# Kernel optimization log

Measured on AMD Instinct MI355X. Metric: run time of the kernel, lower is better.

## Reference

```python
import jax, jax.numpy as jnp
import numpy as np

N_SIDE = 8
N_PATCHES = 24
W_NORMALS = 1.0
W_PLANAR = 1.0
W_COLLISION = 0.01
W_TEMPLATE = 1.0
W_SYMMETRY = 0.0
SIGMA = 0.1

_lin = np.linspace(0.0, 1.0, N_SIDE).astype(np.float32)
_S, _T = np.meshgrid(_lin, _lin, indexing='ij')
S_GRID = jnp.asarray(_S.flatten())
T_GRID = jnp.asarray(_T.flatten())

def _build_topology():
    n = N_SIDE
    tris = []
    for i in range(n - 1):
        for j in range(n - 1):
            v00 = i * n + j; v10 = (i + 1) * n + j
            v01 = i * n + j + 1; v11 = (i + 1) * n + j + 1
            tris.append([v00, v10, v01]); tris.append([v10, v11, v01])
    tris = np.array(tris, dtype=np.int32)
    edges_pts = np.array([
        [i * n + 0 for i in range(n)],        # edge 0: t=0
        [(n - 1) * n + j for j in range(n)],  # edge 1: s=1
        [i * n + (n - 1) for i in range(n)],  # edge 2: t=1
        [0 * n + j for j in range(n)],        # edge 3: s=0
    ], dtype=np.int32)
    edges_tris = []
    for e in edges_pts:
        es = set(int(x) for x in e)
        et = [ti for ti, t in enumerate(tris) if len(es.intersection(int(v) for v in t)) >= 2]
        edges_tris.append(et[: n - 1])
    return tris, edges_pts, np.array(edges_tris, dtype=np.int32)

TRIANGULATION, GRID_POINT_EDGES, TRIANGULATION_EDGES = _build_topology()

ADJ_PAIRS = [(i, (i + 1) % N_PATCHES, 1) for i in range(N_PATCHES)]
_adjset = set(tuple(sorted((i, (i + 1) % N_PATCHES))) for i in range(N_PATCHES))
NONADJ_PAIRS = [(i, j) for i in range(N_PATCHES) for j in range(i + 1, N_PATCHES)
                if (i, j) not in _adjset]


def _bez_basis(u):
    return jnp.stack([(1 - u) ** 3, 3 * u * (1 - u) ** 2, 3 * u ** 2 * (1 - u), u ** 3], -1)


def coons_sample(s, t, patches):
    """patches [b,P,12,3] cubic-Bezier loop; returns [b,P,M,3]."""
    cp = patches
    c0 = cp[..., 0:4, :]
    c1 = cp[..., 3:7, :]
    c2 = cp[..., 6:10, :]
    c3 = jnp.concatenate([cp[..., 9:12, :], cp[..., 0:1, :]], axis=-2)
    cb = jnp.einsum('mk,bpkc->bpmc', _bez_basis(s), c0)
    cr = jnp.einsum('mk,bpkc->bpmc', _bez_basis(t), c1)
    ct = jnp.einsum('mk,bpkc->bpmc', _bez_basis(1 - s), c2)
    cl = jnp.einsum('mk,bpkc->bpmc', _bez_basis(1 - t), c3)
    P00 = cp[..., 0, :][:, :, None]; P10 = cp[..., 3, :][:, :, None]
    P11 = cp[..., 6, :][:, :, None]; P01 = cp[..., 9, :][:, :, None]
    s_ = s[None, None, :, None]; t_ = t[None, None, :, None]
    ruled = (1 - t_) * cb + t_ * ct + (1 - s_) * cl + s_ * cr
    bil = ((1 - s_) * (1 - t_) * P00 + s_ * (1 - t_) * P10
           + s_ * t_ * P11 + (1 - s_) * t_ * P01)
    return ruled - bil


def _pt_tri_sqdist(p, a, b, c):
    ab = b - a; ac = c - a; ap = p - a
    d1 = jnp.sum(ab * ap, -1); d2 = jnp.sum(ac * ap, -1)
    bp = p - b; d3 = jnp.sum(ab * bp, -1); d4 = jnp.sum(ac * bp, -1)
    cp = p - c; d5 = jnp.sum(ab * cp, -1); d6 = jnp.sum(ac * cp, -1)
    vc = d1 * d4 - d3 * d2; vb = d5 * d2 - d1 * d6; va = d3 * d6 - d5 * d4
    eps = 1e-12
    safe = lambda x: jnp.where(jnp.abs(x) < eps, eps, x)
    t_ab = jnp.clip(d1 / safe(d1 - d3), 0, 1)[..., None]
    t_ac = jnp.clip(d2 / safe(d2 - d6), 0, 1)[..., None]
    t_bc = jnp.clip((d4 - d3) / safe((d4 - d3) + (d5 - d6)), 0, 1)[..., None]
    denom = safe(va + vb + vc)
    v = (vb / denom)[..., None]; w = (vc / denom)[..., None]
    close = a + ab * v + ac * w
    close = jnp.where(((va <= 0) & ((d4 - d3) >= 0) & ((d5 - d6) >= 0))[..., None], b + (c - b) * t_bc, close)
    close = jnp.where(((vb <= 0) & (d2 >= 0) & (d6 <= 0))[..., None], a + ac * t_ac, close)
    close = jnp.where(((d6 >= 0) & (d5 <= d6))[..., None], c, close)
    close = jnp.where(((vc <= 0) & (d1 >= 0) & (d3 <= 0))[..., None], a + ab * t_ab, close)
    close = jnp.where(((d3 >= 0) & (d4 <= d3))[..., None], b, close)
    close = jnp.where(((d1 <= 0) & (d2 <= 0))[..., None], a, close)
    return jnp.sum((p - close) ** 2, -1)


def d_points_to_tris(points, tris):
    """points [K,P,3], tris [K,T,3,3] -> min distance per K."""
    p = points[:, :, None, :]
    a = tris[:, None, :, 0, :]; b = tris[:, None, :, 1, :]; c = tris[:, None, :, 2, :]
    d2 = _pt_tri_sqdist(p, a, b, c)  # [K,P,T]
    return jnp.sqrt(jnp.min(d2, axis=(1, 2)) + 1e-12)


def bboxes_intersect(p1, p2):
    """p1 [b,K,P,3], p2 [b,K,Q,3] -> [b,K] bool."""
    mn1 = p1.min(2); mx1 = p1.max(2); mn2 = p2.min(2); mx2 = p2.max(2)
    return jnp.all((mx1 >= mn2) & (mx2 >= mn1), -1)


def compute_chamfer_losses(points, normals, tp, tn):
    d = (jnp.sum(points ** 2, -1)[:, :, None] + jnp.sum(tp ** 2, -1)[:, None, :]
         - 2 * jnp.einsum('bnc,bmc->bnm', points, tp))
    ca = jnp.min(d, 2); ia = jnp.argmin(d, 2)
    cb = jnp.min(d, 1); ib = jnp.argmin(d, 1)
    na = jnp.sum((normals - jnp.take_along_axis(tn, ia[..., None], 1)) ** 2, -1)
    nb = jnp.sum((tn - jnp.take_along_axis(normals, ib[..., None], 1)) ** 2, -1)
    return ca, cb, na, nb


def planar_patch_loss(st, points, mtds):
    """st [M,2], points [b,P,M,3], mtds [b,P,M]: residual of best-fit linear map."""
    A = jnp.concatenate([st, jnp.ones_like(st[:, :1])], 1)  # [M,3]
    AtA = A.T @ A
    sol = jnp.linalg.solve(AtA, jnp.einsum('mk,bpmc->bpkc', A, points))
    res = points - jnp.einsum('mk,bpkc->bpmc', A, sol)
    l = jnp.sum(res ** 2, -1)
    return jnp.mean(jnp.sum(mtds * l, -1) / jnp.sum(mtds, -1))


def _gather2(x, idx):
    """x [b,K,N,...], idx [K,R] -> x gathered along axis 2."""
    full = idx.reshape((1,) + idx.shape + (1,) * (x.ndim - 3))
    full = jnp.broadcast_to(full, x.shape[:2] + (idx.shape[1],) + x.shape[3:])
    return jnp.take_along_axis(x, full, axis=2)


def _forward(target, patches, points, normals, mtds, st, template_normals):
    b, n_patches = patches.shape[0], patches.shape[1]
    target_points = target[:, :, :3]
    target_normals = target[:, :, 3:]
    pts_flat = points.reshape(b, -1, 3)
    nrm_flat = normals.reshape(b, -1, 3)
    mtds_flat = mtds.reshape(b, -1)

    ca, cb, na, nb = compute_chamfer_losses(pts_flat, nrm_flat, target_points, target_normals)
    ca = jnp.sum(mtds_flat * ca, -1) / jnp.sum(mtds_flat, -1)
    cb = cb.mean(1)
    chamfer_loss = ((ca + cb).mean() / 2).reshape(1)
    na = jnp.sum(mtds_flat * na, -1) / jnp.sum(mtds_flat, -1)
    nb = nb.mean(-1)
    normals_loss = ((na + nb).mean() / 2).reshape(1)

    tnl = jnp.sum((template_normals[None] - normals) ** 2, -1)  # [b,P,M]
    template_normals_loss = (jnp.sum(mtds * tnl, -1) / jnp.sum(mtds, -1)).mean().reshape(1)

    planar_loss = planar_patch_loss(st, points, mtds).reshape(1)

    # ---- collision ----
    tri_idx = jnp.asarray(TRIANGULATION)
    grid_points = coons_sample(S_GRID, T_GRID, patches)       # [b,P,64,3]
    triangles = grid_points[:, :, tri_idx]                    # [b,P,98,3,3]

    i1s, i2s, e1s = zip(*ADJ_PAIRS)
    i1s = np.array(i1s); i2s = np.array(i2s); e1s = np.array(e1s)
    K = len(e1s)
    pts1 = _gather2(grid_points[:, i1s], jnp.asarray(GRID_POINT_EDGES[e1s]))    # [b,K,8,3]
    tris1 = _gather2(triangles[:, i1s], jnp.asarray(TRIANGULATION_EDGES[e1s]))  # [b,K,7,3,3]
    pts2 = grid_points[:, i2s]
    tris2 = triangles[:, i2s]
    mask_adj = bboxes_intersect(pts1, pts2).any(0)  # [K]
    d1 = d_points_to_tris(pts1.reshape(b * K, 8, 3), tris2.reshape(b * K, -1, 3, 3))
    d2 = d_points_to_tris(pts2.reshape(b * K, -1, 3), tris1.reshape(b * K, -1, 3, 3))
    d = jnp.minimum(d1, d2).reshape(b, K)
    col_adj = jnp.where(mask_adj[None, :], jnp.exp(-(d / SIGMA) ** 2), 0.0)

    j1s, j2s = zip(*NONADJ_PAIRS)
    j1s = np.array(j1s); j2s = np.array(j2s)
    Kn = len(j1s)
    p1 = grid_points[:, j1s]; p2 = grid_points[:, j2s]
    t1 = triangles[:, j1s]; t2 = triangles[:, j2s]
    mask_non = bboxes_intersect(p1, p2).any(0)  # [Kn]
    d1 = d_points_to_tris(p1.reshape(b * Kn, -1, 3), t2.reshape(b * Kn, -1, 3, 3))
    d2 = d_points_to_tris(p2.reshape(b * Kn, -1, 3), t1.reshape(b * Kn, -1, 3, 3))
    dn = jnp.minimum(d1, d2).reshape(b, Kn)
    col_non = jnp.where(mask_non[None, :], jnp.exp(-(dn / SIGMA) ** 2), 0.0)

    collision_loss = (col_adj.sum(-1) + col_non.sum(-1)).mean().reshape(1)
    symmetry_loss = jnp.zeros(1, dtype=patches.dtype)

    loss = (chamfer_loss + W_NORMALS * normals_loss + W_COLLISION * collision_loss
            + W_PLANAR * planar_loss + W_TEMPLATE * template_normals_loss
            + W_SYMMETRY * symmetry_loss)
    return (loss, chamfer_loss, normals_loss, collision_loss, planar_loss,
            template_normals_loss, symmetry_loss)


def setup_inputs() -> dict:
    key = jax.random.key(0)
    ks = jax.random.split(key, 7)
    b, P, M, Mt = 4, N_PATCHES, 256, 4096
    return {
        'target': jax.random.normal(ks[0], (b, Mt, 6), jnp.float32),
        'patches': jax.random.normal(ks[1], (b, P, 12, 3), jnp.float32),
        'points': jax.random.normal(ks[2], (b, P, M, 3), jnp.float32),
        'normals': jax.random.normal(ks[3], (b, P, M, 3), jnp.float32),
        'mtds': jax.random.uniform(ks[4], (b, P, M), jnp.float32) + 0.01,
        'st': jax.random.uniform(ks[5], (M, 2), jnp.float32),
        'template_normals': jax.random.normal(ks[6], (P, M, 3), jnp.float32),
    }


def reference(target, patches, points, normals, mtds, st, template_normals):
    return _forward(target, patches, points, normals, mtds, st, template_normals)
```

## Files before the change

### kernel.cpp

```cpp
#include <hip/hip_runtime.h>
#include <math.h>

#define NPATCH 24
#define NB 4
#define MPTS 256
#define MT 4096
#define NPTS (NPATCH*MPTS)
#define GRIDPTS 64
#define SIGMA2INV 100.0f
#define PRUNE_MARGIN 0.45f


__device__ inline unsigned encodeFloat(float f) {
    unsigned u = __float_as_uint(f);
    return (u & 0x80000000u) ? ~u : (u | 0x80000000u);
}
__device__ inline float decodeFloat(unsigned e) {
    return __uint_as_float((e & 0x80000000u) ? (e ^ 0x80000000u) : ~e);
}

__device__ inline unsigned long long waveMinU64(unsigned long long k) {
    for (int o = 32; o > 0; o >>= 1) {
        unsigned long long other = __shfl_xor(k, o);
        k = (other < k) ? other : k;
    }
    return k;
}

template<int NV>
__device__ inline void blockReduceSumN(const float* vals, float* out, float* scratch) {
    int wid = threadIdx.x >> 6, lane = threadIdx.x & 63;
#pragma unroll
    for (int i = 0; i < NV; ++i) {
        float v = vals[i];
        for (int o = 32; o > 0; o >>= 1) v += __shfl_down(v, o);
        if (lane == 0) scratch[wid * NV + i] = v;
    }
    __syncthreads();
    if (threadIdx.x < NV)
        out[threadIdx.x] = scratch[0 * NV + threadIdx.x] + scratch[1 * NV + threadIdx.x] +
                           scratch[2 * NV + threadIdx.x] + scratch[3 * NV + threadIdx.x];
    __syncthreads();
}

__device__ inline float clamp01f(float x) { return fminf(fmaxf(x, 0.0f), 1.0f); }
__device__ inline float safercp(float x) {
    float s = fabsf(x) < 1e-12f ? 1e-12f : x;
    return __builtin_amdgcn_rcpf(s);
}

__device__ inline float ptTriSqDistP(float px, float py, float pz, const float4* T) {
    float4 f0 = T[0], f1 = T[1], f2 = T[2], f3 = T[3];
    float ax = f0.x, ay = f0.y, az = f0.z;
    float abx = f1.x, aby = f1.y, abz = f1.z;
    float acx = f2.x, acy = f2.y, acz = f2.z;
    float abp = abx * px + aby * py + abz * pz;
    float acp = acx * px + acy * py + acz * pz;
    float d1 = abp - f0.w;
    float d2 = acp - f1.w;
    float d3 = abp - f2.w;
    float d4 = acp - f3.x;
    float d5 = abp - f3.y;
    float d6 = acp - f3.z;
    float vc = d1 * d4 - d3 * d2;
    float vb = d5 * d2 - d1 * d6;
    float va = d3 * d6 - d5 * d4;
    float t_ab = clamp01f(d1 * safercp(d1 - d3));
    float t_ac = clamp01f(d2 * safercp(d2 - d6));
    float t_bc = clamp01f((d4 - d3) * safercp((d4 - d3) + (d5 - d6)));
    float rden = safercp(va + vb + vc);
    float v = vb * rden, w = vc * rden;
    float clx = ax + abx * v + acx * w;
    float cly = ay + aby * v + acy * w;
    float clz = az + abz * v + acz * w;
    if (va <= 0.0f && (d4 - d3) >= 0.0f && (d5 - d6) >= 0.0f) {
        clx = (ax + abx) + (acx - abx) * t_bc;
        cly = (ay + aby) + (acy - aby) * t_bc;
        clz = (az + abz) + (acz - abz) * t_bc;
    }
    if (vb <= 0.0f && d2 >= 0.0f && d6 <= 0.0f) {
        clx = ax + acx * t_ac; cly = ay + acy * t_ac; clz = az + acz * t_ac;
    }
    if (d6 >= 0.0f && d5 <= d6) { clx = ax + acx; cly = ay + acy; clz = az + acz; }
    if (vc <= 0.0f && d1 >= 0.0f && d3 <= 0.0f) {
        clx = ax + abx * t_ab; cly = ay + aby * t_ab; clz = az + abz * t_ab;
    }
    if (d3 >= 0.0f && d4 <= d3) { clx = ax + abx; cly = ay + aby; clz = az + abz; }
    if (d1 <= 0.0f && d2 <= 0.0f) { clx = ax; cly = ay; clz = az; }
    float dx = px - clx, dy = py - cly, dz = pz - clz;
    return dx * dx + dy * dy + dz * dz;
}

__global__ __launch_bounds__(128) void k_coons_tri(const float* __restrict__ patches,
                                                   float* __restrict__ grid,
                                                   float* __restrict__ bbF,
                                                   float* __restrict__ bbE,
                                                   float4* __restrict__ TDg,
                                                   float4* __restrict__ TSg,
                                                   unsigned* __restrict__ pairmin,
                                                   float* __restrict__ acc) {
    __shared__ float Pl[192];
    int bp = blockIdx.x;
    int m = threadIdx.x;
    if (bp == 0) {
        for (int i = m; i < 1104; i += 128) pairmin[i] = 0xFFFFFFFFu;
        if (m < 32) acc[m] = 0.0f;
    }
    if (m < 64) {
        int i = m >> 3, j = m & 7;
        float s = (i == 7) ? 1.0f : (float)i * (1.0f / 7.0f);
        float t = (j == 7) ? 1.0f : (float)j * (1.0f / 7.0f);
        const float* cp = patches + bp * 36;
        float bs[4], bt[4], bs1[4], bt1[4];
        {
            float u, vv;
            u = s; vv = 1.0f - u; bs[0] = vv * vv * vv; bs[1] = 3.f * u * vv * vv; bs[2] = 3.f * u * u * vv; bs[3] = u * u * u;
            u = t; vv = 1.0f - u; bt[0] = vv * vv * vv; bt[1] = 3.f * u * vv * vv; bt[2] = 3.f * u * u * vv; bt[3] = u * u * u;
            u = 1.0f - s; vv = 1.0f - u; bs1[0] = vv * vv * vv; bs1[1] = 3.f * u * vv * vv; bs1[2] = 3.f * u * u * vv; bs1[3] = u * u * u;
            u = 1.0f - t; vv = 1.0f - u; bt1[0] = vv * vv * vv; bt1[1] = 3.f * u * vv * vv; bt1[2] = 3.f * u * u * vv; bt1[3] = u * u * u;
        }
        float g[3];
#pragma unroll
        for (int c = 0; c < 3; ++c) {
            float cb = bs[0] * cp[0 * 3 + c] + bs[1] * cp[1 * 3 + c] + bs[2] * cp[2 * 3 + c] + bs[3] * cp[3 * 3 + c];
            float cr = bt[0] * cp[3 * 3 + c] + bt[1] * cp[4 * 3 + c] + bt[2] * cp[5 * 3 + c] + bt[3] * cp[6 * 3 + c];
            float ct = bs1[0] * cp[6 * 3 + c] + bs1[1] * cp[7 * 3 + c] + bs1[2] * cp[8 * 3 + c] + bs1[3] * cp[9 * 3 + c];
            float cl = bt1[0] * cp[9 * 3 + c] + bt1[1] * cp[10 * 3 + c] + bt1[2] * cp[11 * 3 + c] + bt1[3] * cp[0 * 3 + c];
            float P00 = cp[0 * 3 + c], P10 = cp[3 * 3 + c], P11 = cp[6 * 3 + c], P01 = cp[9 * 3 + c];
            float ruled = (1.0f - t) * cb + t * ct + (1.0f - s) * cl + s * cr;
            float bil = (1.0f - s) * (1.0f - t) * P00 + s * (1.0f - t) * P10 + s * t * P11 + (1.0f - s) * t * P01;
            g[c] = ruled - bil;
            grid[(bp * GRIDPTS + m) * 3 + c] = g[c];
            Pl[m * 3 + c] = g[c];
        }
        float mnF[3], mxF[3], mnE[3], mxE[3];
        bool edge = (m >= 56);
#pragma unroll
        for (int c = 0; c < 3; ++c) {
            mnF[c] = g[c]; mxF[c] = g[c];
            mnE[c] = edge ? g[c] : 1e30f;
            mxE[c] = edge ? g[c] : -1e30f;
        }
        for (int o = 32; o > 0; o >>= 1) {
#pragma unroll
            for (int c = 0; c < 3; ++c) {
                mnF[c] = fminf(mnF[c], __shfl_down(mnF[c], o));
                mxF[c] = fmaxf(mxF[c], __shfl_down(mxF[c], o));
                mnE[c] = fminf(mnE[c], __shfl_down(mnE[c], o));
                mxE[c] = fmaxf(mxE[c], __shfl_down(mxE[c], o));
            }
        }
        if (m == 0) {
#pragma unroll
            for (int c = 0; c < 3; ++c) {
                bbF[bp * 6 + c] = mnF[c]; bbF[bp * 6 + 3 + c] = mxF[c];
                bbE[bp * 6 + c] = mnE[c]; bbE[bp * 6 + 3 + c] = mxE[c];
            }
        }
    }
    __syncthreads();
    int t = m;
    if (t < 98) {
        int cell = t >> 1, ii = cell / 7, jj = cell - ii * 7;
        int v00 = ii * 8 + jj;
        int va, vb, vc;
        if (t & 1) { va = v00 + 8; vb = v00 + 9; vc = v00 + 1; }
        else       { va = v00;     vb = v00 + 8; vc = v00 + 1; }
        float ax = Pl[va * 3], ay = Pl[va * 3 + 1], az = Pl[va * 3 + 2];
        float bx = Pl[vb * 3], by = Pl[vb * 3 + 1], bz = Pl[vb * 3 + 2];
        float cx = Pl[vc * 3], cy = Pl[vc * 3 + 1], cz = Pl[vc * 3 + 2];
        float abx = bx - ax, aby = by - ay, abz = bz - az;
        float acx = cx - ax, acy = cy - ay, acz = cz - az;
        float ab_a = abx * ax + aby * ay + abz * az;
        float ac_a = acx * ax + acy * ay + acz * az;
        float ab_b = abx * bx + aby * by + abz * bz;
        float ac_b = acx * bx + acy * by + acz * bz;
        float ab_c = abx * cx + aby * cy + abz * cz;
        float ac_c = acx * cx + acy * cy + acz * cz;
        float4* dst = TDg + ((size_t)bp * 98 + t) * 4;
        dst[0] = make_float4(ax, ay, az, ab_a);
        dst[1] = make_float4(abx, aby, abz, ac_a);
        dst[2] = make_float4(acx, acy, acz, ab_b);
        dst[3] = make_float4(ac_b, ab_c, ac_c, 0.0f);
        float gx = (ax + bx + cx) * (1.0f / 3.0f);
        float gy = (ay + by + cy) * (1.0f / 3.0f);
        float gz = (az + bz + cz) * (1.0f / 3.0f);
        float ra = (ax - gx) * (ax - gx) + (ay - gy) * (ay - gy) + (az - gz) * (az - gz);
        float rb = (bx - gx) * (bx - gx) + (by - gy) * (by - gy) + (bz - gz) * (bz - gz);
        float rc = (cx - gx) * (cx - gx) + (cy - gy) * (cy - gy) + (cz - gz) * (cz - gz);
        float r = sqrtf(fmaxf(ra, fmaxf(rb, rc)));
        TSg[(size_t)bp * 98 + t] = make_float4(gx, gy, gz, r);
    }
}

__global__ __launch_bounds__(256) void k_mega(const float* __restrict__ target,
                                              const float* __restrict__ points,
                                              const float* __restrict__ grid,
                                              const float4* __restrict__ TDg,
                                              const float4* __restrict__ TSg,
                                              const float* __restrict__ bbF,
                                              const float* __restrict__ bbE,
                                              float* __restrict__ pa,
                                              float* __restrict__ pb,
                                              unsigned* __restrict__ pairmin) {
    __shared__ float4 smem[128];
    __shared__ float4 Pts[64];
    __shared__ float4 Sph[98];
    __shared__ unsigned short wl[6272];
    __shared__ int cnt;
    __shared__ float sred[4];
    int id = blockIdx.x;
    int b = blockIdx.y;
    int tid = threadIdx.x;

    if (id >= 528) {
        bool isA = (id < 624);
        int qbase, ch;
        float qx0, qy0, qz0, qx1, qy1, qz1, qx2, qy2, qz2, qx3, qy3, qz3;
        float qx4, qy4, qz4, qx5, qy5, qz5, qx6, qy6, qz6, qx7, qy7, qz7;
        if (isA) {
            int rel = id - 528;
            int qb = rel >> 5; ch = rel & 31;
            qbase = qb * 2048 + tid * 8;
            int chbase = ch * 128;
            if (tid < 128) {
                const float* tp = target + (size_t)(b * MT + chbase + tid) * 6;
                float x = tp[0], y = tp[1], z = tp[2];
                smem[tid] = make_float4(x, y, z, 0.5f * (x * x + y * y + z * z));
            }
            const float4* pf = (const float4*)(points + ((size_t)b * NPTS + qbase) * 3);
            float4 v0 = pf[0], v1 = pf[1], v2 = pf[2], v3 = pf[3], v4 = pf[4], v5 = pf[5];
            qx0 = v0.x; qy0 = v0.y; qz0 = v0.z;
            qx1 = v0.w; qy1 = v1.x; qz1 = v1.y;
            qx2 = v1.z; qy2 = v1.w; qz2 = v2.x;
            qx3 = v2.y; qy3 = v2.z; qz3 = v2.w;
            qx4 = v3.x; qy4 = v3.y; qz4 = v3.z;
            qx5 = v3.w; qy5 = v4.x; qz5 = v4.y;
            qx6 = v4.z; qy6 = v4.w; qz6 = v5.x;
            qx7 = v5.y; qy7 = v5.z; qz7 = v5.w;
        } else {
            int rel = id - 624;
            int qb = rel / 48; ch = rel - qb * 48;
            qbase = qb * 2048 + tid * 8;
            int chbase = ch * 128;
            if (tid < 128) {
                const float* pp = points + (size_t)(b * NPTS + chbase + tid) * 3;
                float x = pp[0], y = pp[1], z = pp[2];
                smem[tid] = make_float4(x, y, z, 0.5f * (x * x + y * y + z * z));
            }
            const float* tf = target + (size_t)(b * MT + qbase) * 6;
            float2 a0 = *(const float2*)(tf + 0);  float z0 = tf[2];
            float2 a1 = *(const float2*)(tf + 6);  float z1 = tf[8];
            float2 a2 = *(const float2*)(tf + 12); float z2 = tf[14];
            float2 a3 = *(const float2*)(tf + 18); float z3 = tf[20];
            float2 a4 = *(const float2*)(tf + 24); float z4 = tf[26];
            float2 a5 = *(const float2*)(tf + 30); float z5 = tf[32];
            float2 a6 = *(const float2*)(tf + 36); float z6 = tf[38];
            float2 a7 = *(const float2*)(tf + 42); float z7 = tf[44];
            qx0 = a0.x; qy0 = a0.y; qz0 = z0;
            qx1 = a1.x; qy1 = a1.y; qz1 = z1;
            qx2 = a2.x; qy2 = a2.y; qz2 = z2;
            qx3 = a3.x; qy3 = a3.y; qz3 = z3;
            qx4 = a4.x; qy4 = a4.y; qz4 = z4;
            qx5 = a5.x; qy5 = a5.y; qz5 = z5;
            qx6 = a6.x; qy6 = a6.y; qz6 = z6;
            qx7 = a7.x; qy7 = a7.y; qz7 = z7;
        }
        __syncthreads();
        float sc0 = 1e30f, sc1 = 1e30f, sc2 = 1e30f, sc3 = 1e30f;
        float sc4 = 1e30f, sc5 = 1e30f, sc6 = 1e30f, sc7 = 1e30f;
#pragma unroll 8
        for (int k = 0; k < 128; ++k) {
            float4 T = smem[k];
            sc0 = fminf(sc0, fmaf(-qx0, T.x, fmaf(-qy0, T.y, fmaf(-qz0, T.z, T.w))));
            sc1 = fminf(sc1, fmaf(-qx1, T.x, fmaf(-qy1, T.y, fmaf(-qz1, T.z, T.w))));
            sc2 = fminf(sc2, fmaf(-qx2, T.x, fmaf(-qy2, T.y, fmaf(-qz2, T.z, T.w))));
            sc3 = fminf(sc3, fmaf(-qx3, T.x, fmaf(-qy3, T.y, fmaf(-qz3, T.z, T.w))));
            sc4 = fminf(sc4, fmaf(-qx4, T.x, fmaf(-qy4, T.y, fmaf(-qz4, T.z, T.w))));
            sc5 = fminf(sc5, fmaf(-qx5, T.x, fmaf(-qy5, T.y, fmaf(-qz5, T.z, T.w))));
            sc6 = fminf(sc6, fmaf(-qx6, T.x, fmaf(-qy6, T.y, fmaf(-qz6, T.z, T.w))));
            sc7 = fminf(sc7, fmaf(-qx7, T.x, fmaf(-qy7, T.y, fmaf(-qz7, T.z, T.w))));
        }
        float* dstp = isA ? (pa + ((size_t)(b * 32 + ch)) * NPTS + qbase)
                          : (pb + ((size_t)(b * 48 + ch)) * MT + qbase);
        *(float4*)(dstp) = make_float4(sc0, sc1, sc2, sc3);
        *(float4*)(dstp + 4) = make_float4(sc4, sc5, sc6, sc7);
        return;
    }

    float best = 1e30f;
    int pairIdx;

    if (id < 24) {
        int pair = id;
        pairIdx = pair;
        int i1 = pair, i2 = (pair + 1) % NPATCH;
        bool mask = false;
        for (int bb = 0; bb < NB; ++bb) {
            const float* B1 = bbE + (bb * NPATCH + i1) * 6;
            const float* B2 = bbF + (bb * NPATCH + i2) * 6;
            bool it = (B1[3] >= B2[0]) && (B2[3] >= B1[0]) &&
                      (B1[4] >= B2[1]) && (B2[4] >= B1[1]) &&
                      (B1[5] >= B2[2]) && (B2[5] >= B1[2]);
            mask |= it;
        }
        if (!mask) return;
        const float* P1 = grid + (size_t)(b * NPATCH + i1) * 192;
        const float* P2 = grid + (size_t)(b * NPATCH + i2) * 192;
        const float4* T1 = TDg + (size_t)(b * NPATCH + i1) * 98 * 4;
        const float4* T2 = TDg + (size_t)(b * NPATCH + i2) * 98 * 4;
        for (int tt = tid; tt < 1232; tt += 256) {
            const float4* T;
            float px, py, pz;
            if (tt < 784) {
                int ptI = tt / 98, tri = tt - ptI * 98;
                const float* gp = P1 + (56 + ptI) * 3;
                px = gp[0]; py = gp[1]; pz = gp[2];
                T = T2 + tri * 4;
            } else {
                int rr = tt - 784;
                int ptI = rr / 7, e = rr - ptI * 7;
                const float* gp = P2 + ptI * 3;
                px = gp[0]; py = gp[1]; pz = gp[2];
                T = T1 + (85 + 2 * e) * 4;
            }
            best = fminf(best, ptTriSqDistP(px, py, pz, T));
        }
    } else {
        int r = id - 24;
        int pi2 = r >> 1, dir = r & 1;
        pairIdx = 24 + pi2;
        int k = pi2, i1 = 0;
        while (i1 < NPATCH) {
            int cnt_ = (i1 == 0) ? 21 : (22 - i1);
            if (k < cnt_) break;
            k -= cnt_; ++i1;
        }
        int i2 = i1 + 2 + k;
        bool mask = false;
        for (int bb = 0; bb < NB; ++bb) {
            const float* B1 = bbF + (bb * NPATCH + i1) * 6;
            const float* B2 = bbF + (bb * NPATCH + i2) * 6;
            bool it = (B1[3] >= B2[0]) && (B2[3] >= B1[0]) &&
                      (B1[4] >= B2[1]) && (B2[4] >= B1[1]) &&
                      (B1[5] >= B2[2]) && (B2[5] >= B1[2]);
            mask |= it;
        }
        if (!mask) return;
        int ip_pts = dir ? i2 : i1;
        int ip_tri = dir ? i1 : i2;
        if (tid < 64) {
            const float* gp = grid + ((size_t)(b * NPATCH + ip_pts) * 64 + tid) * 3;
            Pts[tid] = make_float4(gp[0], gp[1], gp[2], 0.0f);
        } else if (tid < 128) {
            int q = tid - 64;
            const float* gq = grid + ((size_t)(b * NPATCH + ip_tri) * 64 + q) * 3;
            smem[q] = make_float4(gq[0], gq[1], gq[2], 0.0f);
        } else if (tid < 226) {
            int t = tid - 128;
            Sph[t] = TSg[(size_t)(b * NPATCH + ip_tri) * 98 + t];
        }
        if (tid == 0) cnt = 0;
        __syncthreads();
        int pt = tid & 63;
        float4 P = Pts[pt];
        float px = P.x, py = P.y, pz = P.z;
        float ub = 1e30f;
        int o0 = (tid >> 6) * 16;
        for (int q = o0; q < o0 + 16; ++q) {
            float4 Q = smem[q];
            float dx = px - Q.x, dy = py - Q.y, dz = pz - Q.z;
            ub = fminf(ub, dx * dx + dy * dy + dz * dz);
        }
        for (int o = 32; o > 0; o >>= 1) ub = fminf(ub, __shfl_xor(ub, o));
        if ((tid & 63) == 0) sred[tid >> 6] = ub;
        __syncthreads();
        ub = fminf(fminf(sred[0], sred[1]), fminf(sred[2], sred[3]));
        float sB = fminf(sqrtf(ub) + 1e-4f, PRUNE_MARGIN);
        best = ub;
        int lane = tid & 63;
        int wtri = tid >> 6;
        for (int t = wtri; t < 98; t += 4) {
            float4 S = Sph[t];
            float dx = px - S.x, dy = py - S.y, dz = pz - S.z;
            float lb = dx * dx + dy * dy + dz * dz;
            float thr = sB + S.w;
            bool pred = (lb <= thr * thr);
            unsigned long long mb = __ballot(pred);
            if (mb != 0ull) {
                int wbase;
                if (lane == 0) wbase = atomicAdd(&cnt, __popcll(mb));
                wbase = __shfl(wbase, 0);
                if (pred) {
                    int off = __popcll(mb & ((1ull << lane) - 1ull));
                    wl[wbase + off] = (unsigned short)((pt << 7) | t);
                }
            }
        }
        __syncthreads();
        int n = cnt;
        const float4* TD = TDg + (size_t)(b * NPATCH + ip_tri) * 98 * 4;
        for (int i = tid; i < n; i += 256) {
            int w = wl[i];
            int ppt = w >> 7, t = w & 127;
            float4 PP = Pts[ppt];
            best = fminf(best, ptTriSqDistP(PP.x, PP.y, PP.z, TD + t * 4));
        }
        __syncthreads();
    }

    for (int o = 32; o > 0; o >>= 1) best = fminf(best, __shfl_down(best, o));
    if ((tid & 63) == 0) sred[tid >> 6] = best;
    __syncthreads();
    if (tid == 0) {
        float d2 = fminf(fminf(sred[0], sred[1]), fminf(sred[2], sred[3]));
        atomicMin(&pairmin[b * 276 + pairIdx], encodeFloat(d2));
    }
}

__global__ __launch_bounds__(256) void k_argmin(const float* __restrict__ target,
                                                const float* __restrict__ points,
                                                const float* __restrict__ pa,
                                                const float* __restrict__ pb,
                                                unsigned long long* __restrict__ best_a,
                                                unsigned long long* __restrict__ best_b) {
    int w = blockIdx.x * 4 + (threadIdx.x >> 6);
    int lane = threadIdx.x & 63;
    if (w < 24576) {
        int b = w / NPTS, qi = w - b * NPTS;
        float v = (lane < 32) ? pa[((size_t)(b * 32 + lane)) * NPTS + qi] : 1e30f;
        unsigned long long key = ((unsigned long long)encodeFloat(v) << 32) | (unsigned)lane;
        key = waveMinU64(key);
        int minch = (int)(key & 0xffffffffu);
        int base = minch * 128;
        const float* pp = points + ((size_t)b * NPTS + qi) * 3;
        float px = pp[0], py = pp[1], pz = pp[2];
        const float* tb0 = target + (size_t)b * MT * 6;
        unsigned long long bk = 0xFFFFFFFFFFFFFFFFull;
#pragma unroll
        for (int rr = 0; rr < 2; ++rr) {
            int k = base + lane + rr * 64;
            const float* tq = tb0 + (size_t)k * 6;
            float x = tq[0], y = tq[1], z = tq[2];
            float hw = 0.5f * (x * x + y * y + z * z);
            float s = fmaf(-px, x, fmaf(-py, y, fmaf(-pz, z, hw)));
            unsigned long long kk = ((unsigned long long)encodeFloat(s) << 32) | (unsigned)k;
            bk = (kk < bk) ? kk : bk;
        }
        bk = waveMinU64(bk);
        if (lane == 0) best_a[(size_t)b * NPTS + qi] = bk;
    } else {
        int idx = w - 24576;
        int b = idx / MT, mt = idx - b * MT;
        float v = (lane < 48) ? pb[((size_t)(b * 48 + lane)) * MT + mt] : 1e30f;
        unsigned long long key = ((unsigned long long)encodeFloat(v) << 32) | (unsigned)lane;
        key = waveMinU64(key);
        int minch = (int)(key & 0xffffffffu);
        int base = minch * 128;
        const float* tq = target + (size_t)(b * MT + mt) * 6;
        float tx = tq[0], ty = tq[1], tz = tq[2];
        const float* pt0 = points + (size_t)b * NPTS * 3;
        unsigned long long bk = 0xFFFFFFFFFFFFFFFFull;
#pragma unroll
        for (int rr = 0; rr < 2; ++rr) {
            int k = base + lane + rr * 64;
            const float* pp2 = pt0 + (size_t)k * 3;
            float x = pp2[0], y = pp2[1], z = pp2[2];
            float hw = 0.5f * (x * x + y * y + z * z);
            float s = fmaf(-tx, x, fmaf(-ty, y, fmaf(-tz, z, hw)));
            unsigned long long kk = ((unsigned long long)encodeFloat(s) << 32) | (unsigned)k;
            bk = (kk < bk) ? kk : bk;
        }
        bk = waveMinU64(bk);
        if (lane == 0) best_b[(size_t)b * MT + mt] = bk;
    }
}

__global__ __launch_bounds__(256) void k_final(const float* __restrict__ points,
                                               const float* __restrict__ normals,
                                               const float* __restrict__ target,
                                               const float* __restrict__ mtds,
                                               const float* __restrict__ st,
                                               const float* __restrict__ tmpl,
                                               const unsigned long long* __restrict__ best_a,
                                               const unsigned long long* __restrict__ best_b,
                                               float* __restrict__ acc) {
    int id = blockIdx.x, b = blockIdx.y;
    if (id < 24) {
        int p = id;
        int m = threadIdx.x;
        int bp = b * NPATCH + p;
        const float* pp = points + (size_t)(bp * MPTS + m) * 3;
        float px = pp[0], py = pp[1], pz = pp[2];
        float pn = px * px + py * py + pz * pz;
        const float* nr = normals + (size_t)(bp * MPTS + m) * 3;
        float nx = nr[0], ny = nr[1], nz = nr[2];
        float w = mtds[bp * MPTS + m];
        float s = st[2 * m], t = st[2 * m + 1];
        unsigned long long pk = best_a[(size_t)b * NPTS + p * MPTS + m];
        float ca = fmaf(2.0f, decodeFloat((unsigned)(pk >> 32)), pn);
        int ia = (int)(pk & 0xffffffffu);
        const float* tq = target + (size_t)(b * MT + ia) * 6 + 3;
        float dx = nx - tq[0], dy = ny - tq[1], dz = nz - tq[2];
        float na = dx * dx + dy * dy + dz * dz;
        const float* tm = tmpl + (size_t)(p * MPTS + m) * 3;
        float ex = tm[0] - nx, ey = tm[1] - ny, ez = tm[2] - nz;
        float tnl = ex * ex + ey * ey + ez * ez;

        float vals[18];
        vals[0] = w * ca; vals[1] = w * na; vals[2] = w; vals[3] = w * tnl;
        vals[4] = s * px; vals[5] = s * py; vals[6] = s * pz;
        vals[7] = t * px; vals[8] = t * py; vals[9] = t * pz;
        vals[10] = px; vals[11] = py; vals[12] = pz;
        vals[13] = s * s; vals[14] = s * t; vals[15] = s; vals[16] = t * t; vals[17] = t;

        __shared__ float scratch[4 * 18];
        __shared__ float red[18];
        blockReduceSumN<18>(vals, red, scratch);

        __shared__ float sol[9];
        __shared__ float smtd_sh;
        if (threadIdx.x == 0) {
            float a00 = red[13], a01 = red[14], a02 = red[15];
            float a11 = red[16], a12 = red[17], a22 = 256.0f;
            float c00 = a11 * a22 - a12 * a12;
            float c01 = a02 * a12 - a01 * a22;
            float c02 = a01 * a12 - a02 * a11;
            float det = a00 * c00 + a01 * c01 + a02 * c02;
            float idet = 1.0f / det;
            float i00 = c00 * idet, i01 = c01 * idet, i02 = c02 * idet;
            float i11 = (a00 * a22 - a02 * a02) * idet;
            float i12 = (a01 * a02 - a00 * a12) * idet;
            float i22 = (a00 * a11 - a01 * a01) * idet;
#pragma unroll
            for (int c = 0; c < 3; ++c) {
                float b0 = red[4 + c], b1 = red[7 + c], b2 = red[10 + c];
                sol[0 * 3 + c] = i00 * b0 + i01 * b1 + i02 * b2;
                sol[1 * 3 + c] = i01 * b0 + i11 * b1 + i12 * b2;
                sol[2 * 3 + c] = i02 * b0 + i12 * b1 + i22 * b2;
            }
            smtd_sh = red[2];
            atomicAdd(&acc[0 + b], red[0]);
            atomicAdd(&acc[4 + b], red[1]);
            atomicAdd(&acc[8 + b], red[2]);
            atomicAdd(&acc[20], red[3] / red[2]);
        }
        __syncthreads();
        float rx = px - (s * sol[0] + t * sol[3] + sol[6]);
        float ry = py - (s * sol[1] + t * sol[4] + sol[7]);
        float rz = pz - (s * sol[2] + t * sol[5] + sol[8]);
        float v2 = w * (rx * rx + ry * ry + rz * rz);
        for (int o = 32; o > 0; o >>= 1) v2 += __shfl_down(v2, o);
        __shared__ float s2[4];
        if ((threadIdx.x & 63) == 0) s2[threadIdx.x >> 6] = v2;
        __syncthreads();
        if (threadIdx.x == 0)
            atomicAdd(&acc[21], (s2[0] + s2[1] + s2[2] + s2[3]) / smtd_sh);
    } else {
        int mc = id - 24;
        int mt = mc * 256 + threadIdx.x;
        const float* tq = target + (size_t)(b * MT + mt) * 6;
        float tx = tq[0], ty = tq[1], tz = tq[2];
        float tn2 = tx * tx + ty * ty + tz * tz;
        unsigned long long pk = best_b[(size_t)b * MT + mt];
        float cb = fmaf(2.0f, decodeFloat((unsigned)(pk >> 32)), tn2);
        int ib = (int)(pk & 0xffffffffu);
        const float* nr = normals + (size_t)(b * NPTS + ib) * 3;
        float dx = tq[3] - nr[0], dy = tq[4] - nr[1], dz = tq[5] - nr[2];
        float nb = dx * dx + dy * dy + dz * dz;
        float vals[2] = {cb, nb};
        __shared__ float scratchB[4 * 2];
        __shared__ float redB[2];
        blockReduceSumN<2>(vals, redB, scratchB);
        if (threadIdx.x == 0) {
            atomicAdd(&acc[12 + b], redB[0]);
            atomicAdd(&acc[16 + b], redB[1]);
        }
    }
}

__global__ __launch_bounds__(256) void k_finish(const float* __restrict__ acc,
                                                const unsigned* __restrict__ pairmin,
                                                float* __restrict__ out) {
    int tid = threadIdx.x;
    float s = 0.0f;
    for (int idx = tid; idx < 4 * 276; idx += 256) {
        unsigned key = pairmin[idx];
        if (key != 0xFFFFFFFFu) {
            float d2 = decodeFloat(key);
            s += expf(-(d2 + 1e-12f) * SIGMA2INV);
        }
    }
    for (int o = 32; o > 0; o >>= 1) s += __shfl_down(s, o);
    __shared__ float sred[4];
    if ((tid & 63) == 0) sred[tid >> 6] = s;
    __syncthreads();
    if (tid == 0) {
        float col = (sred[0] + sred[1] + sred[2] + sred[3]) * 0.25f;
        float ch = 0.0f, no = 0.0f;
        for (int b = 0; b < NB; ++b) {
            float caw = acc[0 + b] / acc[8 + b];
            float naw = acc[4 + b] / acc[8 + b];
            float cbm = acc[12 + b] / (float)MT;
            float nbm = acc[16 + b] / (float)MT;
            ch += caw + cbm;
            no += naw + nbm;
        }
        ch = ch * 0.25f * 0.5f;
        no = no * 0.25f * 0.5f;
        float tpl = acc[20] / 96.0f;
        float pl = acc[21] / 96.0f;
        float loss = ch + no + 0.01f * col + pl + tpl;
        out[0] = loss;
        out[1] = ch;
        out[2] = no;
        out[3] = col;
        out[4] = pl;
        out[5] = tpl;
        out[6] = 0.0f;
    }
}

extern "C" void kernel_launch(void* const* d_in, const int* in_sizes, int n_in,
                              void* d_out, int out_size, void* d_ws, size_t ws_size,
                              hipStream_t stream) {
    (void)in_sizes; (void)n_in; (void)out_size; (void)ws_size;
    const float* target = (const float*)d_in[0];
    const float* patches = (const float*)d_in[1];
    const float* points = (const float*)d_in[2];
    const float* normals = (const float*)d_in[3];
    const float* mtds = (const float*)d_in[4];
    const float* st = (const float*)d_in[5];
    const float* tmpl = (const float*)d_in[6];
    float* out = (float*)d_out;
    char* ws = (char*)d_ws;

    float* grid = (float*)(ws + 0);
    float* bbF = (float*)(ws + 73728);
    float* bbE = (float*)(ws + 76032);
    unsigned* pairmin = (unsigned*)(ws + 78336);
    float* acc = (float*)(ws + 82752);
    float4* TDg = (float4*)(ws + 82880);
    float4* TSg = (float4*)(ws + 684992);
    float* pa = (float*)(ws + 835520);
    float* pb = (float*)(ws + 3981248);
    unsigned long long* best_a = (unsigned long long*)(ws + 7126976);
    unsigned long long* best_b = (unsigned long long*)(ws + 7323584);

    k_coons_tri<<<dim3(NB * NPATCH), dim3(128), 0, stream>>>(patches, grid, bbF, bbE,
                                                             TDg, TSg, pairmin, acc);
    k_mega<<<dim3(720, NB), dim3(256), 0, stream>>>(target, points, grid, TDg, TSg,
                                                    bbF, bbE, pa, pb, pairmin);
    k_argmin<<<dim3(10240), dim3(256), 0, stream>>>(target, points, pa, pb, best_a, best_b);
    k_final<<<dim3(40, NB), dim3(256), 0, stream>>>(points, normals, target, mtds, st,
                                                    tmpl, best_a, best_b, acc);
    k_finish<<<1, 256, 0, stream>>>(acc, pairmin, out);
}
```

Baseline: 75.32 us.

## Remap argmin to one query per lane, add sphere culling, fuse finish

k_argmin is reorganized so each lane owns one query point and the four waves split the channel scan and the 128-candidate refinement, combining partial results through shared memory. This replaces per-query wave reductions and strided target loads with fewer, coalesced blocks. The collision narrow phase gets a bounding-sphere lower-bound test that skips exact point-triangle distance work when it cannot improve the current minimum. k_finish is folded into k_final using a last-block-done atomic counter, which removes one launch but relies on acc[31] being zeroed beforehand and on correct fencing.

```diff
diff --git a/kernel.cpp b/kernel.cpp
--- a/kernel.cpp
+++ b/kernel.cpp
@@ -17,14 +17,6 @@
 }
 __device__ inline float decodeFloat(unsigned e) {
     return __uint_as_float((e & 0x80000000u) ? (e ^ 0x80000000u) : ~e);
-}
-
-__device__ inline unsigned long long waveMinU64(unsigned long long k) {
-    for (int o = 32; o > 0; o >>= 1) {
-        unsigned long long other = __shfl_xor(k, o);
-        k = (other < k) ? other : k;
-    }
-    return k;
 }
 
 template<int NV>
@@ -404,6 +396,11 @@
             int w = wl[i];
             int ppt = w >> 7, t = w & 127;
             float4 PP = Pts[ppt];
+            float4 S = Sph[t];
+            float dx = PP.x - S.x, dy = PP.y - S.y, dz = PP.z - S.z;
+            float lb = dx * dx + dy * dy + dz * dz;
+            float thr = sqrtf(best) + S.w;
+            if (lb > thr * thr) continue;
             best = fminf(best, ptTriSqDistP(PP.x, PP.y, PP.z, TD + t * 4));
         }
         __syncthreads();
@@ -424,55 +421,102 @@
                                                 const float* __restrict__ pb,
                                                 unsigned long long* __restrict__ best_a,
                                                 unsigned long long* __restrict__ best_b) {
-    int w = blockIdx.x * 4 + (threadIdx.x >> 6);
-    int lane = threadIdx.x & 63;
-    if (w < 24576) {
-        int b = w / NPTS, qi = w - b * NPTS;
-        float v = (lane < 32) ? pa[((size_t)(b * 32 + lane)) * NPTS + qi] : 1e30f;
-        unsigned long long key = ((unsigned long long)encodeFloat(v) << 32) | (unsigned)lane;
-        key = waveMinU64(key);
-        int minch = (int)(key & 0xffffffffu);
-        int base = minch * 128;
-        const float* pp = points + ((size_t)b * NPTS + qi) * 3;
+    __shared__ unsigned long long red[4][64];
+    int blk = blockIdx.x;
+    int tid = threadIdx.x;
+    int lane = tid & 63, grp = tid >> 6;
+    if (blk < 384) {
+        int Q0 = blk * 64;
+        int b = Q0 / NPTS, q0 = Q0 - b * NPTS;
+        int q = q0 + lane;
+        unsigned long long k1 = 0xFFFFFFFFFFFFFFFFull;
+        const float* paB = pa + (size_t)b * 32 * NPTS + q;
+#pragma unroll
+        for (int c = 0; c < 8; ++c) {
+            int ch = grp * 8 + c;
+            float v = paB[(size_t)ch * NPTS];
+            unsigned long long kk = ((unsigned long long)encodeFloat(v) << 32) | (unsigned)ch;
+            k1 = (kk < k1) ? kk : k1;
+        }
+        red[grp][lane] = k1;
+        __syncthreads();
+        unsigned long long m0 = red[0][lane], m1 = red[1][lane];
+        unsigned long long m2 = red[2][lane], m3 = red[3][lane];
+        unsigned long long mm = m0 < m1 ? m0 : m1;
+        mm = m2 < mm ? m2 : mm;
+        mm = m3 < mm ? m3 : mm;
+        int minch = (int)(mm & 0xffffffffu);
+        int base = minch * 128 + grp * 32;
+        const float* pp = points + ((size_t)b * NPTS + q) * 3;
         float px = pp[0], py = pp[1], pz = pp[2];
         const float* tb0 = target + (size_t)b * MT * 6;
         unsigned long long bk = 0xFFFFFFFFFFFFFFFFull;
-#pragma unroll
-        for (int rr = 0; rr < 2; ++rr) {
-            int k = base + lane + rr * 64;
-            const float* tq = tb0 + (size_t)k * 6;
+        for (int c = 0; c < 32; ++c) {
+            int kidx = base + c;
+            const float* tq = tb0 + (size_t)kidx * 6;
             float x = tq[0], y = tq[1], z = tq[2];
             float hw = 0.5f * (x * x + y * y + z * z);
             float s = fmaf(-px, x, fmaf(-py, y, fmaf(-pz, z, hw)));
-            unsigned long long kk = ((unsigned long long)encodeFloat(s) << 32) | (unsigned)k;
+            unsigned long long kk = ((unsigned long long)encodeFloat(s) << 32) | (unsigned)kidx;
             bk = (kk < bk) ? kk : bk;
         }
-        bk = waveMinU64(bk);
-        if (lane == 0) best_a[(size_t)b * NPTS + qi] = bk;
+        __syncthreads();
+        red[grp][lane] = bk;
+        __syncthreads();
+        if (tid < 64) {
+            unsigned long long r0 = red[0][tid], r1 = red[1][tid];
+            unsigned long long r2 = red[2][tid], r3 = red[3][tid];
+            unsigned long long rr = r0 < r1 ? r0 : r1;
+            rr = r2 < rr ? r2 : rr;
+            rr = r3 < rr ? r3 : rr;
+            best_a[(size_t)b * NPTS + q0 + tid] = rr;
+        }
     } else {
-        int idx = w - 24576;
-        int b = idx / MT, mt = idx - b * MT;
-        float v = (lane < 48) ? pb[((size_t)(b * 48 + lane)) * MT + mt] : 1e30f;
-        unsigned long long key = ((unsigned long long)encodeFloat(v) << 32) | (unsigned)lane;
-        key = waveMinU64(key);
-        int minch = (int)(key & 0xffffffffu);
-        int base = minch * 128;
+        int Q0 = (blk - 384) * 64;
+        int b = Q0 / MT, m0q = Q0 - b * MT;
+        int mt = m0q + lane;
+        unsigned long long k1 = 0xFFFFFFFFFFFFFFFFull;
+        const float* pbB = pb + (size_t)b * 48 * MT + mt;
+#pragma unroll
+        for (int c = 0; c < 12; ++c) {
+            int ch = grp * 12 + c;
+            float v = pbB[(size_t)ch * MT];
+            unsigned long long kk = ((unsigned long long)encodeFloat(v) << 32) | (unsigned)ch;
+            k1 = (kk < k1) ? kk : k1;
+        }
+        red[grp][lane] = k1;
+        __syncthreads();
+        unsigned long long m0 = red[0][lane], m1 = red[1][lane];
+        unsigned long long m2 = red[2][lane], m3 = red[3][lane];
+        unsigned long long mm = m0 < m1 ? m0 : m1;
+        mm = m2 < mm ? m2 : mm;
+        mm = m3 < mm ? m3 : mm;
+        int minch = (int)(mm & 0xffffffffu);
+        int base = minch * 128 + grp * 32;
         const float* tq = target + (size_t)(b * MT + mt) * 6;
         float tx = tq[0], ty = tq[1], tz = tq[2];
         const float* pt0 = points + (size_t)b * NPTS * 3;
         unsigned long long bk = 0xFFFFFFFFFFFFFFFFull;
-#pragma unroll
-        for (int rr = 0; rr < 2; ++rr) {
-            int k = base + lane + rr * 64;
-            const float* pp2 = pt0 + (size_t)k * 3;
+        for (int c = 0; c < 32; ++c) {
+            int kidx = base + c;
+            const float* pp2 = pt0 + (size_t)kidx * 3;
             float x = pp2[0], y = pp2[1], z = pp2[2];
             float hw = 0.5f * (x * x + y * y + z * z);
             float s = fmaf(-tx, x, fmaf(-ty, y, fmaf(-tz, z, hw)));
-            unsigned long long kk = ((unsigned long long)encodeFloat(s) << 32) | (unsigned)k;
+            unsigned long long kk = ((unsigned long long)encodeFloat(s) << 32) | (unsigned)kidx;
             bk = (kk < bk) ? kk : bk;
         }
-        bk = waveMinU64(bk);
-        if (lane == 0) best_b[(size_t)b * MT + mt] = bk;
+        __syncthreads();
+        red[grp][lane] = bk;
+        __syncthreads();
+        if (tid < 64) {
+            unsigned long long r0 = red[0][tid], r1 = red[1][tid];
+            unsigned long long r2 = red[2][tid], r3 = red[3][tid];
+            unsigned long long rr = r0 < r1 ? r0 : r1;
+            rr = r2 < rr ? r2 : rr;
+            rr = r3 < rr ? r3 : rr;
+            best_b[(size_t)b * MT + m0q + tid] = rr;
+        }
     }
 }
 
@@ -484,7 +528,11 @@
                                                const float* __restrict__ tmpl,
                                                const unsigned long long* __restrict__ best_a,
                                                const unsigned long long* __restrict__ best_b,
-                                               float* __restrict__ acc) {
+                                               float* __restrict__ acc,
+                                               unsigned* __restrict__ pairmin,
+                                               float* __restrict__ out) {
+    __shared__ float finred[4];
+    __shared__ int lastFlag;
     int id = blockIdx.x, b = blockIdx.y;
     if (id < 24) {
         int p = id;
@@ -577,39 +625,44 @@
             atomicAdd(&acc[16 + b], redB[1]);
         }
     }
-}
-
-__global__ __launch_bounds__(256) void k_finish(const float* __restrict__ acc,
-                                                const unsigned* __restrict__ pairmin,
-                                                float* __restrict__ out) {
+
+    __syncthreads();
+    if (threadIdx.x == 0) {
+        __threadfence();
+        unsigned done = atomicAdd((unsigned*)acc + 31, 1u) + 1u;
+        lastFlag = (done == 160u) ? 1 : 0;
+    }
+    __syncthreads();
+    if (!lastFlag) return;
+    __threadfence();
     int tid = threadIdx.x;
     float s = 0.0f;
     for (int idx = tid; idx < 4 * 276; idx += 256) {
-        unsigned key = pairmin[idx];
+        unsigned key = atomicOr(&pairmin[idx], 0u);
         if (key != 0xFFFFFFFFu) {
             float d2 = decodeFloat(key);
             s += expf(-(d2 + 1e-12f) * SIGMA2INV);
         }
     }
     for (int o = 32; o > 0; o >>= 1) s += __shfl_down(s, o);
-    __shared__ float sred[4];
-    if ((tid & 63) == 0) sred[tid >> 6] = s;
+    if ((tid & 63) == 0) finred[tid >> 6] = s;
     __syncthreads();
     if (tid == 0) {
-        float col = (sred[0] + sred[1] + sred[2] + sred[3]) * 0.25f;
+        float col = (finred[0] + finred[1] + finred[2] + finred[3]) * 0.25f;
         float ch = 0.0f, no = 0.0f;
-        for (int b = 0; b < NB; ++b) {
-            float caw = acc[0 + b] / acc[8 + b];
-            float naw = acc[4 + b] / acc[8 + b];
-            float cbm = acc[12 + b] / (float)MT;
-            float nbm = acc[16 + b] / (float)MT;
-            ch += caw + cbm;
-            no += naw + nbm;
+        for (int bb = 0; bb < NB; ++bb) {
+            float sa = atomicAdd(&acc[0 + bb], 0.0f);
+            float sna = atomicAdd(&acc[4 + bb], 0.0f);
+            float sw = atomicAdd(&acc[8 + bb], 0.0f);
+            float scb = atomicAdd(&acc[12 + bb], 0.0f);
+            float snb = atomicAdd(&acc[16 + bb], 0.0f);
+            ch += sa / sw + scb / (float)MT;
+            no += sna / sw + snb / (float)MT;
         }
         ch = ch * 0.25f * 0.5f;
         no = no * 0.25f * 0.5f;
-        float tpl = acc[20] / 96.0f;
-        float pl = acc[21] / 96.0f;
+        float tpl = atomicAdd(&acc[20], 0.0f) / 96.0f;
+        float pl = atomicAdd(&acc[21], 0.0f) / 96.0f;
         float loss = ch + no + 0.01f * col + pl + tpl;
         out[0] = loss;
         out[1] = ch;
@@ -651,8 +704,7 @@
                                                              TDg, TSg, pairmin, acc);
     k_mega<<<dim3(720, NB), dim3(256), 0, stream>>>(target, points, grid, TDg, TSg,
                                                     bbF, bbE, pa, pb, pairmin);
-    k_argmin<<<dim3(10240), dim3(256), 0, stream>>>(target, points, pa, pb, best_a, best_b);
+    k_argmin<<<dim3(640), dim3(256), 0, stream>>>(target, points, pa, pb, best_a, best_b);
     k_final<<<dim3(40, NB), dim3(256), 0, stream>>>(points, normals, target, mtds, st,
-                                                    tmpl, best_a, best_b, acc);
-    k_finish<<<1, 256, 0, stream>>>(acc, pairmin, out);
-}
+                                                    tmpl, best_a, best_b, acc, pairmin, out);
+}
```

Measured after the change: 79.66 us. 5.8% more time.

## Derive target-to-point column minima from point-to-target distance tiles

Applied to the files above, without the earlier changes.

The chamfer partial-min blocks now compute the point-to-target distance tile once and obtain both directions from it. Row minima stay in registers, and column minima come from a 16-lane shuffle reduction stored in a shared buffer aliased with the worklist. This removes the separate 96 target-query blocks per batch. The cost is extra shuffles and min operations in the inner loop, plus a second shared-memory write-out phase.

```diff
diff --git a/kernel.cpp b/kernel.cpp
--- a/kernel.cpp
+++ b/kernel.cpp
@@ -206,85 +206,71 @@
     __shared__ float4 smem[128];
     __shared__ float4 Pts[64];
     __shared__ float4 Sph[98];
-    __shared__ unsigned short wl[6272];
     __shared__ int cnt;
     __shared__ float sred[4];
+    __shared__ __attribute__((aligned(16))) unsigned char poolbuf[12544];
+    float (*colsh)[132] = (float(*)[132])poolbuf;
+    unsigned short* wl = (unsigned short*)poolbuf;
     int id = blockIdx.x;
     int b = blockIdx.y;
     int tid = threadIdx.x;
 
     if (id >= 528) {
-        bool isA = (id < 624);
-        int qbase, ch;
-        float qx0, qy0, qz0, qx1, qy1, qz1, qx2, qy2, qz2, qx3, qy3, qz3;
-        float qx4, qy4, qz4, qx5, qy5, qz5, qx6, qy6, qz6, qx7, qy7, qz7;
-        if (isA) {
-            int rel = id - 528;
-            int qb = rel >> 5; ch = rel & 31;
-            qbase = qb * 2048 + tid * 8;
-            int chbase = ch * 128;
-            if (tid < 128) {
-                const float* tp = target + (size_t)(b * MT + chbase + tid) * 6;
-                float x = tp[0], y = tp[1], z = tp[2];
-                smem[tid] = make_float4(x, y, z, 0.5f * (x * x + y * y + z * z));
-            }
-            const float4* pf = (const float4*)(points + ((size_t)b * NPTS + qbase) * 3);
-            float4 v0 = pf[0], v1 = pf[1], v2 = pf[2], v3 = pf[3], v4 = pf[4], v5 = pf[5];
-            qx0 = v0.x; qy0 = v0.y; qz0 = v0.z;
-            qx1 = v0.w; qy1 = v1.x; qz1 = v1.y;
-            qx2 = v1.z; qy2 = v1.w; qz2 = v2.x;
-            qx3 = v2.y; qy3 = v2.z; qz3 = v2.w;
-            qx4 = v3.x; qy4 = v3.y; qz4 = v3.z;
-            qx5 = v3.w; qy5 = v4.x; qz5 = v4.y;
-            qx6 = v4.z; qy6 = v4.w; qz6 = v5.x;
-            qx7 = v5.y; qy7 = v5.z; qz7 = v5.w;
-        } else {
-            int rel = id - 624;
-            int qb = rel / 48; ch = rel - qb * 48;
-            qbase = qb * 2048 + tid * 8;
-            int chbase = ch * 128;
-            if (tid < 128) {
-                const float* pp = points + (size_t)(b * NPTS + chbase + tid) * 3;
-                float x = pp[0], y = pp[1], z = pp[2];
-                smem[tid] = make_float4(x, y, z, 0.5f * (x * x + y * y + z * z));
-            }
-            const float* tf = target + (size_t)(b * MT + qbase) * 6;
-            float2 a0 = *(const float2*)(tf + 0);  float z0 = tf[2];
-            float2 a1 = *(const float2*)(tf + 6);  float z1 = tf[8];
-            float2 a2 = *(const float2*)(tf + 12); float z2 = tf[14];
-            float2 a3 = *(const float2*)(tf + 18); float z3 = tf[20];
-            float2 a4 = *(const float2*)(tf + 24); float z4 = tf[26];
-            float2 a5 = *(const float2*)(tf + 30); float z5 = tf[32];
-            float2 a6 = *(const float2*)(tf + 36); float z6 = tf[38];
-            float2 a7 = *(const float2*)(tf + 42); float z7 = tf[44];
-            qx0 = a0.x; qy0 = a0.y; qz0 = z0;
-            qx1 = a1.x; qy1 = a1.y; qz1 = z1;
-            qx2 = a2.x; qy2 = a2.y; qz2 = z2;
-            qx3 = a3.x; qy3 = a3.y; qz3 = z3;
-            qx4 = a4.x; qy4 = a4.y; qz4 = z4;
-            qx5 = a5.x; qy5 = a5.y; qz5 = z5;
-            qx6 = a6.x; qy6 = a6.y; qz6 = z6;
-            qx7 = a7.x; qy7 = a7.y; qz7 = z7;
-        }
+        int rel = id - 528;
+        int qb = rel >> 5, ch = rel & 31;
+        int qbase = qb * 2048 + tid * 8;
+        int chbase = ch * 128;
+        if (tid < 128) {
+            const float* tp = target + (size_t)(b * MT + chbase + tid) * 6;
+            float x = tp[0], y = tp[1], z = tp[2];
+            smem[tid] = make_float4(x, y, z, 0.5f * (x * x + y * y + z * z));
+        }
+        const float4* pf = (const float4*)(points + ((size_t)b * NPTS + qbase) * 3);
+        float4 v0 = pf[0], v1 = pf[1], v2 = pf[2], v3 = pf[3], v4 = pf[4], v5 = pf[5];
+        float qx0 = v0.x, qy0 = v0.y, qz0 = v0.z;
+        float qx1 = v0.w, qy1 = v1.x, qz1 = v1.y;
+        float qx2 = v1.z, qy2 = v1.w, qz2 = v2.x;
+        float qx3 = v2.y, qy3 = v2.z, qz3 = v2.w;
+        float qx4 = v3.x, qy4 = v3.y, qz4 = v3.z;
+        float qx5 = v3.w, qy5 = v4.x, qz5 = v4.y;
+        float qx6 = v4.z, qy6 = v4.w, qz6 = v5.x;
+        float qx7 = v5.y, qy7 = v5.z, qz7 = v5.w;
         __syncthreads();
         float sc0 = 1e30f, sc1 = 1e30f, sc2 = 1e30f, sc3 = 1e30f;
         float sc4 = 1e30f, sc5 = 1e30f, sc6 = 1e30f, sc7 = 1e30f;
-#pragma unroll 8
+        int sub = tid >> 4;
+        bool cw = ((tid & 15) == 0);
+#pragma unroll 4
         for (int k = 0; k < 128; ++k) {
             float4 T = smem[k];
-            sc0 = fminf(sc0, fmaf(-qx0, T.x, fmaf(-qy0, T.y, fmaf(-qz0, T.z, T.w))));
-            sc1 = fminf(sc1, fmaf(-qx1, T.x, fmaf(-qy1, T.y, fmaf(-qz1, T.z, T.w))));
-            sc2 = fminf(sc2, fmaf(-qx2, T.x, fmaf(-qy2, T.y, fmaf(-qz2, T.z, T.w))));
-            sc3 = fminf(sc3, fmaf(-qx3, T.x, fmaf(-qy3, T.y, fmaf(-qz3, T.z, T.w))));
-            sc4 = fminf(sc4, fmaf(-qx4, T.x, fmaf(-qy4, T.y, fmaf(-qz4, T.z, T.w))));
-            sc5 = fminf(sc5, fmaf(-qx5, T.x, fmaf(-qy5, T.y, fmaf(-qz5, T.z, T.w))));
-            sc6 = fminf(sc6, fmaf(-qx6, T.x, fmaf(-qy6, T.y, fmaf(-qz6, T.z, T.w))));
-            sc7 = fminf(sc7, fmaf(-qx7, T.x, fmaf(-qy7, T.y, fmaf(-qz7, T.z, T.w))));
-        }
-        float* dstp = isA ? (pa + ((size_t)(b * 32 + ch)) * NPTS + qbase)
-                          : (pb + ((size_t)(b * 48 + ch)) * MT + qbase);
+            float s0 = fmaf(-qx0, T.x, fmaf(-qy0, T.y, fmaf(-qz0, T.z, T.w)));
+            float s1 = fmaf(-qx1, T.x, fmaf(-qy1, T.y, fmaf(-qz1, T.z, T.w)));
+            float s2 = fmaf(-qx2, T.x, fmaf(-qy2, T.y, fmaf(-qz2, T.z, T.w)));
+            float s3 = fmaf(-qx3, T.x, fmaf(-qy3, T.y, fmaf(-qz3, T.z, T.w)));
+            float s4 = fmaf(-qx4, T.x, fmaf(-qy4, T.y, fmaf(-qz4, T.z, T.w)));
+            float s5 = fmaf(-qx5, T.x, fmaf(-qy5, T.y, fmaf(-qz5, T.z, T.w)));
+            float s6 = fmaf(-qx6, T.x, fmaf(-qy6, T.y, fmaf(-qz6, T.z, T.w)));
+            float s7 = fmaf(-qx7, T.x, fmaf(-qy7, T.y, fmaf(-qz7, T.z, T.w)));
+            sc0 = fminf(sc0, s0); sc1 = fminf(sc1, s1);
+            sc2 = fminf(sc2, s2); sc3 = fminf(sc3, s3);
+            sc4 = fminf(sc4, s4); sc5 = fminf(sc5, s5);
+            sc6 = fminf(sc6, s6); sc7 = fminf(sc7, s7);
+            float cm = fminf(fminf(fminf(s0, s1), fminf(s2, s3)),
+                             fminf(fminf(s4, s5), fminf(s6, s7)));
+            cm = fminf(cm, __shfl_xor(cm, 1));
+            cm = fminf(cm, __shfl_xor(cm, 2));
+            cm = fminf(cm, __shfl_xor(cm, 4));
+            cm = fminf(cm, __shfl_xor(cm, 8));
+            if (cw) colsh[sub][k] = cm;
+        }
+        float* dstp = pa + ((size_t)(b * 32 + ch)) * NPTS + qbase;
         *(float4*)(dstp) = make_float4(sc0, sc1, sc2, sc3);
         *(float4*)(dstp + 4) = make_float4(sc4, sc5, sc6, sc7);
+        __syncthreads();
+        for (int idx = tid; idx < 2048; idx += 256) {
+            int su = idx >> 7, kk = idx & 127;
+            pb[((size_t)(b * 48 + qb * 16 + su)) * MT + chbase + kk] = colsh[su][kk];
+        }
         return;
     }
 
@@ -649,7 +635,7 @@
 
     k_coons_tri<<<dim3(NB * NPATCH), dim3(128), 0, stream>>>(patches, grid, bbF, bbE,
                                                              TDg, TSg, pairmin, acc);
-    k_mega<<<dim3(720, NB), dim3(256), 0, stream>>>(target, points, grid, TDg, TSg,
+    k_mega<<<dim3(624, NB), dim3(256), 0, stream>>>(target, points, grid, TDg, TSg,
                                                     bbF, bbE, pa, pb, pairmin);
     k_argmin<<<dim3(10240), dim3(256), 0, stream>>>(target, points, pa, pb, best_a, best_b);
     k_final<<<dim3(40, NB), dim3(256), 0, stream>>>(points, normals, target, mtds, st,
```

Result: slower. 89.37 us (+18.7%).
